# Performance work log

Hardware: AMD Instinct MI355X
Metric: run time of the kernel (lower is better)

Reference implementation:

```python
import jax, jax.numpy as jnp
import numpy as np

N, D = 128, 512  # batch, hypercube dim (in_features == n_2d_layers == out_features)

def setup_inputs() -> dict:
    key = jax.random.key(0)
    k1, k2, k3 = jax.random.split(key, 3)
    bound = 1.0 / np.sqrt(D)
    x = jax.random.normal(k1, (N, D, D), dtype=jnp.float32)
    # kaiming_uniform_(a=sqrt(5)) on (in, layers, out) ~ U(-1/sqrt(fan_in), 1/sqrt(fan_in)) scale
    w = jax.random.uniform(k2, (D, D, D), dtype=jnp.float32, minval=-bound, maxval=bound)
    b = jax.random.uniform(k3, (D, D), dtype=jnp.float32, minval=-bound, maxval=bound)
    return {"x": x, "w": w, "b": b}

def reference(x, w, b):
    # Original: (x.expand((L, *x.shape)).movedim(0,-2) * w).sum(-1) + b
    # which reduces to out[n,i,j] = sum_k x[n,i,k] * w[i,j,k] + b[i,j]
    # (w axes: (in_features, n_2d_layers, out_features), all equal D)
    return jnp.einsum('nik,ijk->nij', x, w) + b
```

## Files before the change

### kernel.cpp

```cpp
#include <hip/hip_runtime.h>


#define Dd 512
#define DD (512 * 512)

typedef __attribute__((ext_vector_type(8))) short bf16x8;
typedef __attribute__((ext_vector_type(4))) short bf16x4;
typedef __attribute__((ext_vector_type(4))) float f32x4;

__device__ __forceinline__ short f2bf(float f) {
    unsigned u = __builtin_bit_cast(unsigned, f);
    u += 0x7FFFu + ((u >> 16) & 1u);
    return (short)(u >> 16);
}

__device__ __forceinline__ bf16x8 cvt8(float4 a, float4 b) {
    bf16x8 h;
    h[0] = f2bf(a.x); h[1] = f2bf(a.y); h[2] = f2bf(a.z); h[3] = f2bf(a.w);
    h[4] = f2bf(b.x); h[5] = f2bf(b.y); h[6] = f2bf(b.z); h[7] = f2bf(b.w);
    return h;
}

__device__ __forceinline__ void glds16(const float* g, float* l) {
    __builtin_amdgcn_global_load_lds(
        (const __attribute__((address_space(1))) void*)g,
        (__attribute__((address_space(3))) void*)l, 16, 0, 0);
}

__global__ __launch_bounds__(512, 4)
void linear3d_kernel(const float* __restrict__ x,
                     const float* __restrict__ w,
                     const float* __restrict__ b,
                     float* __restrict__ out) {
    const int i    = blockIdx.x;
    const int tid  = threadIdx.x;
    const int lane = tid & 63;
    const int wid  = tid >> 6;
    const int row16 = lane & 15;
    const int cg    = lane >> 4;

    __shared__ float f32r[2][8192];
    __shared__ short b16s[8192];

    const float* xi = x + (size_t)i * Dd;
    const float* wi = w + (size_t)i * DD;

#define CVTW(V, q) do {                                                        \
    int row_  = 2 * wid + ((q) >> 1);                                          \
    int byte_ = (row_ * 1024 + ((q) & 1) * 512 + lane * 8) ^ ((row_ & 7) << 4);\
    bf16x4 h_ = { f2bf(V.x), f2bf(V.y), f2bf(V.z), f2bf(V.w) };                \
    *(bf16x4*)((char*)b16s + byte_) = h_;                                      \
} while (0)

    float bias_cur = b[i * Dd + row16];
    #pragma unroll
    for (int q = 0; q < 4; ++q) { int t = wid * 4 + q;
        glds16(wi + t * 256 + lane * 4, &f32r[0][t * 256]); }
    #pragma unroll
    for (int q = 0; q < 4; ++q) { int t = wid * 4 + q;
        glds16(wi + 8192 + t * 256 + lane * 4, &f32r[1][t * 256]); }
    asm volatile("" ::: "memory");

    const float* xrow = xi + (size_t)(wid * 16 + row16) * DD + cg * 8;
    float4 pa0 = *(const float4*)(xrow + 0);
    float4 pa1 = *(const float4*)(xrow + 4);
    float4 pa2 = *(const float4*)(xrow + 32);
    float4 pa3 = *(const float4*)(xrow + 36);

    asm volatile("s_waitcnt vmcnt(8)" ::: "memory");
    __builtin_amdgcn_sched_barrier(0);
    {
        float4 v0 = *(const float4*)(&f32r[0][wid * 1024 +   0 + lane * 4]);
        float4 v1 = *(const float4*)(&f32r[0][wid * 1024 + 256 + lane * 4]);
        float4 v2 = *(const float4*)(&f32r[0][wid * 1024 + 512 + lane * 4]);
        float4 v3 = *(const float4*)(&f32r[0][wid * 1024 + 768 + lane * 4]);
        CVTW(v0, 0); CVTW(v1, 1); CVTW(v2, 2); CVTW(v3, 3);
    }

    bf16x8 xf[16];
    #pragma unroll
    for (int r = 0; r < 8; ++r) {
        float4 pb0, pb1, pb2, pb3;
        if (r < 7) {
            const float* xb = xrow + (2 * r + 2) * 32;
            pb0 = *(const float4*)(xb + 0);
            pb1 = *(const float4*)(xb + 4);
            pb2 = *(const float4*)(xb + 32);
            pb3 = *(const float4*)(xb + 36);
        }
        if (r < 7) asm volatile("s_waitcnt vmcnt(4)" ::: "memory");
        else       asm volatile("s_waitcnt vmcnt(0)" ::: "memory");
        __builtin_amdgcn_sched_barrier(0);
        xf[2 * r]     = cvt8(pa0, pa1);
        xf[2 * r + 1] = cvt8(pa2, pa3);
        pa0 = pb0; pa1 = pb1; pa2 = pb2; pa3 = pb3;
    }

    asm volatile("s_waitcnt lgkmcnt(0)" ::: "memory");
    #pragma unroll
    for (int q = 0; q < 4; ++q) { int t = wid * 4 + q;
        glds16(wi + 2 * 8192 + t * 256 + lane * 4, &f32r[0][t * 256]); }
    __builtin_amdgcn_s_barrier();
    __builtin_amdgcn_sched_barrier(0);

#define BODY(c, VMSTR, DO_GLDS, DO_CONV, DO_BIAS) do {                         \
    if (DO_GLDS) {                                                             \
        const float* gs_ = wi + (size_t)((c) + 2) * 8192;                      \
        float* lb_ = &f32r[(c) & 1][0];                                        \
        _Pragma("unroll")                                                      \
        for (int q = 0; q < 4; ++q) { int t_ = wid * 4 + q;                    \
            glds16(gs_ + t_ * 256 + lane * 4, lb_ + t_ * 256); }               \
    }                                                                          \
    float biasN_ = bias_cur;                                                   \
    if (DO_BIAS) biasN_ = b[i * Dd + ((c) + 1) * 16 + row16];                  \
    f32x4 accA = {0.f, 0.f, 0.f, 0.f}, accB = {0.f, 0.f, 0.f, 0.f};            \
    _Pragma("unroll")                                                          \
    for (int s = 0; s < 16; s += 2) {                                          \
        int byA_ = (row16 * 1024 + s * 64 + cg * 16) ^ ((row16 & 7) << 4);     \
        int byB_ = (row16 * 1024 + (s + 1) * 64 + cg * 16) ^ ((row16 & 7) << 4);\
        bf16x8 wfA_ = *(const bf16x8*)((const char*)b16s + byA_);              \
        bf16x8 wfB_ = *(const bf16x8*)((const char*)b16s + byB_);              \
        accA = __builtin_amdgcn_mfma_f32_16x16x32_bf16(xf[s], wfA_, accA, 0, 0, 0);       \
        accB = __builtin_amdgcn_mfma_f32_16x16x32_bf16(xf[s + 1], wfB_, accB, 0, 0, 0);   \
    }                                                                          \
    { int j_ = (c) * 16 + row16;                                               \
      _Pragma("unroll")                                                        \
      for (int r_ = 0; r_ < 4; ++r_) {                                         \
          int n_ = wid * 16 + cg * 4 + r_;                                     \
          out[(size_t)i * Dd + (size_t)n_ * DD + j_] =                         \
              accA[r_] + accB[r_] + bias_cur;                                  \
      } }                                                                      \
    if (DO_CONV) {                                                             \
        asm volatile("s_waitcnt " VMSTR ::: "memory");                         \
        __builtin_amdgcn_sched_barrier(0);                                     \
        const float* fb_ = &f32r[((c) + 1) & 1][0];                            \
        float4 v0_ = *(const float4*)(fb_ + wid * 1024 +   0 + lane * 4);      \
        float4 v1_ = *(const float4*)(fb_ + wid * 1024 + 256 + lane * 4);      \
        float4 v2_ = *(const float4*)(fb_ + wid * 1024 + 512 + lane * 4);      \
        float4 v3_ = *(const float4*)(fb_ + wid * 1024 + 768 + lane * 4);      \
        asm volatile("" ::: "memory");                                         \
        __builtin_amdgcn_s_barrier();     \
        __builtin_amdgcn_sched_barrier(0);                                     \
        CVTW(v0_, 0); CVTW(v1_, 1); CVTW(v2_, 2); CVTW(v3_, 3);                \
        asm volatile("s_waitcnt lgkmcnt(0)" ::: "memory");                     \
        __builtin_amdgcn_s_barrier();                \
        __builtin_amdgcn_sched_barrier(0);                                     \
    }                                                                          \
    bias_cur = biasN_;                                                         \
} while (0)

    BODY(0, "vmcnt(9)", false, true, true);
    #pragma unroll 1
    for (int c = 1; c <= 29; ++c)
        BODY(c, "vmcnt(13)", true, true, true);
    BODY(30, "vmcnt(9)", false, true, true);
    BODY(31, "vmcnt(0)", false, false, false);

#undef BODY
#undef CVTW
}

extern "C" void kernel_launch(void* const* d_in, const int* in_sizes, int n_in,
                              void* d_out, int out_size, void* d_ws, size_t ws_size,
                              hipStream_t stream) {
    const float* x = (const float*)d_in[0];
    const float* w = (const float*)d_in[1];
    const float* b = (const float*)d_in[2];
    float* out = (float*)d_out;
    linear3d_kernel<<<dim3(Dd), dim3(512), 0, stream>>>(x, w, b, out);
}
```

Before: 218.0 us.

## Convert weights to bf16 in place within the f32 staging buffer and drop a barrier

Removes the separate bf16 LDS buffer. Each wave now converts its own slice of the fp32 staging buffer to bf16 in place, and the MFMA loop reads weight fragments from that buffer. This cuts LDS use and one block-wide barrier per chunk. In exchange, the prefetch of chunk c+2 is issued only after the conversion barrier, which shortens how far ahead global-to-LDS loads run.

```diff
diff --git a/kernel.cpp b/kernel.cpp
--- a/kernel.cpp
+++ b/kernel.cpp
@@ -40,42 +40,46 @@
     const int cg    = lane >> 4;
 
     __shared__ float f32r[2][8192];
-    __shared__ short b16s[8192];
 
     const float* xi = x + (size_t)i * Dd;
     const float* wi = w + (size_t)i * DD;
 
-#define CVTW(V, q) do {                                                        \
-    int row_  = 2 * wid + ((q) >> 1);                                          \
-    int byte_ = (row_ * 1024 + ((q) & 1) * 512 + lane * 8) ^ ((row_ & 7) << 4);\
-    bf16x4 h_ = { f2bf(V.x), f2bf(V.y), f2bf(V.z), f2bf(V.w) };                \
-    *(bf16x4*)((char*)b16s + byte_) = h_;                                      \
+#define WGLDS(cidx, slot) do {                                                 \
+    const float* gsrc_ = wi + (size_t)(cidx) * 8192 + wid * 1024;              \
+    float* ldst_ = &f32r[slot][wid * 1024];                                    \
+    _Pragma("unroll")                                                          \
+    for (int q = 0; q < 4; ++q)                                                \
+        glds16(gsrc_ + q * 256 + lane * 4, ldst_ + q * 256);                   \
+} while (0)
+
+#define CONVERT(SLOT) do {                                                     \
+    const float* fb_ = &f32r[SLOT][wid * 1024];                                \
+    float4 c0_ = *(const float4*)(fb_ +   0 + lane * 4);                       \
+    float4 c1_ = *(const float4*)(fb_ + 256 + lane * 4);                       \
+    float4 c2_ = *(const float4*)(fb_ + 512 + lane * 4);                       \
+    float4 c3_ = *(const float4*)(fb_ + 768 + lane * 4);                       \
+    char* wb_ = (char*)&f32r[SLOT][0] + wid * 4096;                            \
+    const int sz0_ = ((2 * wid) & 7) << 4;                                     \
+    const int sz1_ = sz0_ | 16;                                                \
+    bf16x4 h0_ = { f2bf(c0_.x), f2bf(c0_.y), f2bf(c0_.z), f2bf(c0_.w) };       \
+    bf16x4 h1_ = { f2bf(c1_.x), f2bf(c1_.y), f2bf(c1_.z), f2bf(c1_.w) };       \
+    bf16x4 h2_ = { f2bf(c2_.x), f2bf(c2_.y), f2bf(c2_.z), f2bf(c2_.w) };       \
+    bf16x4 h3_ = { f2bf(c3_.x), f2bf(c3_.y), f2bf(c3_.z), f2bf(c3_.w) };       \
+    *(bf16x4*)(wb_ + ((      lane * 8) ^ sz0_)) = h0_;                         \
+    *(bf16x4*)(wb_ + ((512 + lane * 8) ^ sz0_)) = h1_;                         \
+    *(bf16x4*)(wb_ + 1024 + ((      lane * 8) ^ sz1_)) = h2_;                  \
+    *(bf16x4*)(wb_ + 1024 + ((512 + lane * 8) ^ sz1_)) = h3_;                  \
 } while (0)
 
     float bias_cur = b[i * Dd + row16];
-    #pragma unroll
-    for (int q = 0; q < 4; ++q) { int t = wid * 4 + q;
-        glds16(wi + t * 256 + lane * 4, &f32r[0][t * 256]); }
-    #pragma unroll
-    for (int q = 0; q < 4; ++q) { int t = wid * 4 + q;
-        glds16(wi + 8192 + t * 256 + lane * 4, &f32r[1][t * 256]); }
-    asm volatile("" ::: "memory");
+    WGLDS(0, 0);
+    WGLDS(1, 1);
 
     const float* xrow = xi + (size_t)(wid * 16 + row16) * DD + cg * 8;
     float4 pa0 = *(const float4*)(xrow + 0);
     float4 pa1 = *(const float4*)(xrow + 4);
     float4 pa2 = *(const float4*)(xrow + 32);
     float4 pa3 = *(const float4*)(xrow + 36);
-
-    asm volatile("s_waitcnt vmcnt(8)" ::: "memory");
-    __builtin_amdgcn_sched_barrier(0);
-    {
-        float4 v0 = *(const float4*)(&f32r[0][wid * 1024 +   0 + lane * 4]);
-        float4 v1 = *(const float4*)(&f32r[0][wid * 1024 + 256 + lane * 4]);
-        float4 v2 = *(const float4*)(&f32r[0][wid * 1024 + 512 + lane * 4]);
-        float4 v3 = *(const float4*)(&f32r[0][wid * 1024 + 768 + lane * 4]);
-        CVTW(v0, 0); CVTW(v1, 1); CVTW(v2, 2); CVTW(v3, 3);
-    }
 
     bf16x8 xf[16];
     #pragma unroll
@@ -96,68 +100,59 @@
         pa0 = pb0; pa1 = pb1; pa2 = pb2; pa3 = pb3;
     }
 
+    CONVERT(0);
     asm volatile("s_waitcnt lgkmcnt(0)" ::: "memory");
-    #pragma unroll
-    for (int q = 0; q < 4; ++q) { int t = wid * 4 + q;
-        glds16(wi + 2 * 8192 + t * 256 + lane * 4, &f32r[0][t * 256]); }
     __builtin_amdgcn_s_barrier();
     __builtin_amdgcn_sched_barrier(0);
 
-#define BODY(c, VMSTR, DO_GLDS, DO_CONV, DO_BIAS) do {                         \
-    if (DO_GLDS) {                                                             \
-        const float* gs_ = wi + (size_t)((c) + 2) * 8192;                      \
-        float* lb_ = &f32r[(c) & 1][0];                                        \
-        _Pragma("unroll")                                                      \
-        for (int q = 0; q < 4; ++q) { int t_ = wid * 4 + q;                    \
-            glds16(gs_ + t_ * 256 + lane * 4, lb_ + t_ * 256); }               \
-    }                                                                          \
+    const int base_r = (row16 >> 1) * 4096 + (row16 & 1) * 1024;
+    const int swz_r  = (row16 & 7) << 4;
+    const int kx     = cg * 16;
+
+#define BODY(c, DO_CONV, DO_GLDS, DO_BIAS) do {                                \
     float biasN_ = bias_cur;                                                   \
     if (DO_BIAS) biasN_ = b[i * Dd + ((c) + 1) * 16 + row16];                  \
+    const char* buf_ = (const char*)&f32r[(c) & 1][0];                         \
     f32x4 accA = {0.f, 0.f, 0.f, 0.f}, accB = {0.f, 0.f, 0.f, 0.f};            \
     _Pragma("unroll")                                                          \
     for (int s = 0; s < 16; s += 2) {                                          \
-        int byA_ = (row16 * 1024 + s * 64 + cg * 16) ^ ((row16 & 7) << 4);     \
-        int byB_ = (row16 * 1024 + (s + 1) * 64 + cg * 16) ^ ((row16 & 7) << 4);\
-        bf16x8 wfA_ = *(const bf16x8*)((const char*)b16s + byA_);              \
-        bf16x8 wfB_ = *(const bf16x8*)((const char*)b16s + byB_);              \
-        accA = __builtin_amdgcn_mfma_f32_16x16x32_bf16(xf[s], wfA_, accA, 0, 0, 0);       \
-        accB = __builtin_amdgcn_mfma_f32_16x16x32_bf16(xf[s + 1], wfB_, accB, 0, 0, 0);   \
+        bf16x8 wfA_ = *(const bf16x8*)(buf_ + base_r + ((s * 64 + kx) ^ swz_r)); \
+        bf16x8 wfB_ = *(const bf16x8*)(buf_ + base_r + (((s + 1) * 64 + kx) ^ swz_r)); \
+        accA = __builtin_amdgcn_mfma_f32_16x16x32_bf16(xf[s], wfA_, accA, 0, 0, 0);     \
+        accB = __builtin_amdgcn_mfma_f32_16x16x32_bf16(xf[s + 1], wfB_, accB, 0, 0, 0); \
     }                                                                          \
     { int j_ = (c) * 16 + row16;                                               \
       _Pragma("unroll")                                                        \
       for (int r_ = 0; r_ < 4; ++r_) {                                         \
           int n_ = wid * 16 + cg * 4 + r_;                                     \
-          out[(size_t)i * Dd + (size_t)n_ * DD + j_] =                         \
+          out[(size_t)n_ * DD + (size_t)i * Dd + j_] =                         \
               accA[r_] + accB[r_] + bias_cur;                                  \
       } }                                                                      \
     if (DO_CONV) {                                                             \
-        asm volatile("s_waitcnt " VMSTR ::: "memory");                         \
+        asm volatile("s_waitcnt vmcnt(5)" ::: "memory");                       \
         __builtin_amdgcn_sched_barrier(0);                                     \
-        const float* fb_ = &f32r[((c) + 1) & 1][0];                            \
-        float4 v0_ = *(const float4*)(fb_ + wid * 1024 +   0 + lane * 4);      \
-        float4 v1_ = *(const float4*)(fb_ + wid * 1024 + 256 + lane * 4);      \
-        float4 v2_ = *(const float4*)(fb_ + wid * 1024 + 512 + lane * 4);      \
-        float4 v3_ = *(const float4*)(fb_ + wid * 1024 + 768 + lane * 4);      \
-        asm volatile("" ::: "memory");                                         \
-        __builtin_amdgcn_s_barrier();     \
+        CONVERT(((c) + 1) & 1);                                                \
+        asm volatile("s_waitcnt lgkmcnt(0)" ::: "memory");                     \
+        __builtin_amdgcn_s_barrier();                                          \
         __builtin_amdgcn_sched_barrier(0);                                     \
-        CVTW(v0_, 0); CVTW(v1_, 1); CVTW(v2_, 2); CVTW(v3_, 3);                \
-        asm volatile("s_waitcnt lgkmcnt(0)" ::: "memory");                     \
-        __builtin_amdgcn_s_barrier();                \
-        __builtin_amdgcn_sched_barrier(0);                                     \
+        if (DO_GLDS) {                                                         \
+            WGLDS((c) + 2, (c) & 1);                                           \
+            __builtin_amdgcn_sched_barrier(0);                                 \
+        }                                                                      \
     }                                                                          \
     bias_cur = biasN_;                                                         \
 } while (0)
 
-    BODY(0, "vmcnt(9)", false, true, true);
+    BODY(0, true, true, true);
     #pragma unroll 1
     for (int c = 1; c <= 29; ++c)
-        BODY(c, "vmcnt(13)", true, true, true);
-    BODY(30, "vmcnt(9)", false, true, true);
-    BODY(31, "vmcnt(0)", false, false, false);
+        BODY(c, true, true, true);
+    BODY(30, true, false, true);
+    BODY(31, false, false, false);
 
 #undef BODY
-#undef CVTW
+#undef CONVERT
+#undef WGLDS
 }
 
 extern "C" void kernel_launch(void* const* d_in, const int* in_sizes, int n_in,
```

Result: no change. 221.9 us (+1.8%).
